# Performance work log

Hardware: AMD Instinct MI355X
Metric: run time of the kernel (lower is better)

The kernel has to match this reference:

```python
import jax, jax.numpy as jnp
import numpy as np

B, T, C, H, W = 16, 8, 2048, 16, 8
C8, C4, HW, NP = C // 8, C // 4, H * W, T // 2


def _cbr(x, w, s, b):
    # 1x1 conv + folded BN (eval-mode affine) + ReLU; x: (N, Cin, H, W), w: (Cout, Cin)
    y = jnp.einsum('oc,nchw->nohw', w, x)
    return jax.nn.relu(y * s[None, :, None, None] + b[None, :, None, None])


def setup_inputs():
    key = jax.random.key(0)
    ks = jax.random.split(key, 16)
    r = lambda i, shape, sc: jax.random.normal(ks[i], shape, jnp.float32) * sc
    return dict(
        featmap=r(0, (B, T, C, H, W), 1.0),
        re_featmap=r(1, (B * T, C, H, W), 1.0),
        vect_featmap=r(2, (B, T, C), 1.0),
        embed_feat=r(3, (B, T, 128, H, W), 1.0),
        gamma_w=r(4, (C8, C), 0.03), gamma_s=jnp.ones((C8,)), gamma_b=jnp.zeros((C8,)),
        beta_w=r(5, (C8, C), 0.03), beta_s=jnp.ones((C8,)), beta_b=jnp.zeros((C8,)),
        gg_w=r(6, (128, 2 * HW), 0.05), gg_s=jnp.ones((128,)), gg_b=jnp.zeros((128,)),
        tte_w=r(7, (128, 256), 0.05), tte_s=jnp.ones((128,)), tte_b=jnp.zeros((128,)),
        te_w=r(8, (1, 256), 0.05), te_s=jnp.ones((1,)), te_b=jnp.zeros((1,)),
        theta_w=r(9, (C8, C), 0.03), theta_b=jnp.zeros((C8,)),
        cp_w1=r(10, (C8, C4), 0.05), cp_b1=jnp.zeros((C8,)),
        cp_w2=r(11, (C, C8), 0.05), cp_b2=jnp.zeros((C,)),
    )


def reference(featmap, re_featmap, vect_featmap, embed_feat,
              gamma_w, gamma_s, gamma_b, beta_w, beta_s, beta_b,
              gg_w, gg_s, gg_b, tte_w, tte_s, tte_b, te_w, te_s, te_b,
              theta_w, theta_b, cp_w1, cp_b1, cp_w2, cp_b2):
    # spatial attention embeddings: (B, T, C8, HW)
    gamma = _cbr(re_featmap, gamma_w, gamma_s, gamma_b).reshape(B, T, C8, HW)
    beta = _cbr(re_featmap, beta_w, beta_s, beta_b).reshape(B, T, C8, HW)

    # channel attention: Conv1d over time of (B, C, T) -> (B, C8, T)
    cp = jax.nn.relu(jnp.einsum('oc,btc->bot', theta_w, vect_featmap) + theta_b[None, :, None])
    cp = cp.reshape(B, C8, NP, 2)
    c0 = cp[..., 0].transpose(0, 2, 1)  # (B, NP, C8)
    c1 = cp[..., 1].transpose(0, 2, 1)

    def mlp(x):  # (B, NP, C4) -> sigmoid gate (B, NP, C)
        h1 = jax.nn.relu(x @ cp_w1.T + cp_b1)
        return jax.nn.sigmoid(h1 @ cp_w2.T + cp_b2)

    p00 = mlp(jnp.concatenate([c0, c1], -1))  # (B, NP, C)
    p01 = mlp(jnp.concatenate([c1, c0], -1))

    # pairwise spatial graphs
    g0, g1 = gamma[:, 0::2], gamma[:, 1::2]  # (B, NP, C8, HW)
    b0, b1 = beta[:, 0::2], beta[:, 1::2]
    Gs0 = jnp.einsum('bpcs,bpct->bpst', g0, b1)  # (B, NP, HW, HW)
    Gs1 = jnp.einsum('bpcs,bpct->bpst', g1, b0)
    # Gs_in = Gs^T viewed as (HW, H, W); Gs_out = Gs viewed likewise
    j0 = jnp.concatenate([Gs0.transpose(0, 1, 3, 2), Gs1], 2).reshape(B * NP, 2 * HW, H, W)
    j1 = jnp.concatenate([Gs1.transpose(0, 1, 3, 2), Gs0], 2).reshape(B * NP, 2 * HW, H, W)
    gj0 = _cbr(j0, gg_w, gg_s, gg_b)  # (B*NP, 128, H, W)
    gj1 = _cbr(j1, gg_w, gg_s, gg_b)

    ef = embed_feat.reshape(B, NP, 2, 128, H, W)
    e0 = ef[:, :, 0].reshape(B * NP, 128, H, W)
    e1 = ef[:, :, 1].reshape(B * NP, 128, H, W)
    ta = _cbr(jnp.concatenate([e0, e1], 1), tte_w, tte_s, tte_b)  # (B*NP, 128, H, W)
    tb = _cbr(jnp.concatenate([e1, e0], 1), tte_w, tte_s, tte_b)

    def gate(t_feat, gj):  # conv 256->1 + BN + sigmoid
        y = jnp.einsum('oc,nchw->nohw', te_w, jnp.concatenate([t_feat, gj], 1))
        return jax.nn.sigmoid(y * te_s[None, :, None, None] + te_b[None, :, None, None])

    pa = gate(ta, gj0).reshape(B, NP, 1, H, W)
    pb = gate(tb, gj1).reshape(B, NP, 1, H, W)

    f = featmap.reshape(B, NP, 2, C, H, W)
    gate0 = p00[..., None, None] * pa  # (B, NP, C, H, W)
    gate1 = p01[..., None, None] * pb
    out = jax.nn.relu(gate0 * f[:, :, 0] + gate1 * f[:, :, 1])
    return out * out  # (B, T//2, C, H, W)
```

## Files before the change

kernel.cpp:

```cpp
#include <hip/hip_runtime.h>
#include <stdint.h>


typedef _Float16 f16;
typedef _Float16 f16x4 __attribute__((ext_vector_type(4)));
typedef _Float16 f16x8 __attribute__((ext_vector_type(8)));
typedef float f32x4 __attribute__((ext_vector_type(4)));

typedef const void __attribute__((address_space(1)))* gptr1;
typedef void __attribute__((address_space(3)))* lptr3;

__device__ __forceinline__ void gload16(const void* g, void* l) {
  __builtin_amdgcn_global_load_lds((gptr1)g, (lptr3)l, 16, 0, 0);
}

__device__ __forceinline__ float sigmoidf_(float x) { return 1.f / (1.f + expf(-x)); }

#define WAIT_VM6 asm volatile("s_waitcnt vmcnt(6)" ::: "memory")
#define WAIT_VM0 asm volatile("s_waitcnt vmcnt(0)" ::: "memory")
#define WAIT_LGKM8 asm volatile("s_waitcnt lgkmcnt(8)" ::: "memory")
#define WAIT_LGKM0 asm volatile("s_waitcnt lgkmcnt(0)" ::: "memory")

__global__ __launch_bounds__(256) void kPP(const float* __restrict__ x,
                                           f16* __restrict__ Af,
                                           const float* __restrict__ gw, const float* __restrict__ gs,
                                           const float* __restrict__ bw, const float* __restrict__ bs,
                                           const float* __restrict__ gg_w, const float* __restrict__ gg_s,
                                           const float* __restrict__ tte_w, const float* __restrict__ tte_s,
                                           const float* __restrict__ thw, const float* __restrict__ w1,
                                           const float* __restrict__ w2,
                                           f16* __restrict__ Wf,
                                           float* __restrict__ ggT, float* __restrict__ tteT,
                                           float* __restrict__ thwT, float* __restrict__ w1T,
                                           float* __restrict__ w2T) {
  __shared__ __align__(16) char shmem[64 * 129 * 4];
  int t = threadIdx.x;
  int bid = blockIdx.x;
  if (bid < 4096) {
    float (*L)[129] = (float(*)[129])shmem;
    int n = bid >> 5;
    int k0 = (bid & 31) * 64;
    const float* src = x + (size_t)n * 262144 + (size_t)k0 * 128;
    for (int r = 0; r < 8; ++r) {
      int f = r * 256 + t;
      int kk = f >> 5, c4 = (f & 31) * 4;
      float4 v = *(const float4*)(src + kk * 128 + c4);
      L[kk][c4 + 0] = v.x; L[kk][c4 + 1] = v.y; L[kk][c4 + 2] = v.z; L[kk][c4 + 3] = v.w;
    }
    __syncthreads();
    for (int r = 0; r < 4; ++r) {
      int id = r * 256 + t;
      int hw = id >> 3, c = id & 7;
      int cs = c ^ (hw & 7);
      f16x8 h8;
      for (int j = 0; j < 8; ++j)
        h8[j] = (f16)L[cs * 8 + j][hw];
      size_t m = (size_t)n * 128 + hw;
      size_t ob = m * 2048 + (size_t)k0 + (size_t)c * 8;
      *(f16x8*)(Af + ob) = h8;
    }
    return;
  }
  if (bid < 4608) {
    int id = (bid - 4096) * 256 + t;
    int o = id >> 8, cch = id & 255;
    float s; const float* row;
    if (o < 256) { s = gs[o]; row = gw + (size_t)o * 2048; }
    else         { s = bs[o - 256]; row = bw + (size_t)(o - 256) * 2048; }
    int kb = cch >> 3, sub = cch & 7;
    int subd = sub ^ (o & 7);
    f16x8 h8;
    for (int j = 0; j < 8; ++j)
      h8[j] = (f16)(row[cch * 8 + j] * s);
    size_t ob = (size_t)o * 2048 + (size_t)kb * 64 + (size_t)subd * 8;
    *(f16x8*)(Wf + ob) = h8;
    return;
  }
  float (*TL)[65] = (float(*)[65])shmem;
  int tb = bid - 4608;
  const float* src; float* dst; const float* scale = nullptr; int R, C;
  if (tb < 128)      { src = thw;   dst = thwT; R = 256;  C = 2048; }
  else if (tb < 256) { tb -= 128; src = w2;  dst = w2T;  R = 2048; C = 256; }
  else if (tb < 288) { tb -= 256; src = w1;  dst = w1T;  R = 256;  C = 512; }
  else if (tb < 296) { tb -= 288; src = gg_w;  dst = ggT;  scale = gg_s;  R = 128; C = 256; }
  else               { tb -= 296; src = tte_w; dst = tteT; scale = tte_s; R = 128; C = 256; }
  int tpc = C >> 6;
  int r0 = (tb / tpc) * 64, c0 = (tb % tpc) * 64;
  int i16 = t >> 4, j4 = (t & 15) * 4;
  for (int s = 0; s < 4; ++s) {
    int i = i16 + s * 16;
    float4 v = *(const float4*)(src + (size_t)(r0 + i) * C + c0 + j4);
    TL[i][j4 + 0] = v.x; TL[i][j4 + 1] = v.y; TL[i][j4 + 2] = v.z; TL[i][j4 + 3] = v.w;
  }
  __syncthreads();
  for (int s = 0; s < 4; ++s) {
    int j = i16 + s * 16;
    float4 w;
    w.x = TL[j4 + 0][j]; w.y = TL[j4 + 1][j]; w.z = TL[j4 + 2][j]; w.w = TL[j4 + 3][j];
    if (scale) {
      w.x *= scale[r0 + j4 + 0]; w.y *= scale[r0 + j4 + 1];
      w.z *= scale[r0 + j4 + 2]; w.w *= scale[r0 + j4 + 3];
    }
    *(float4*)(dst + (size_t)(c0 + j) * R + r0 + j4) = w;
  }
}

__global__ __launch_bounds__(512, 2) void kGemm8(const f16* __restrict__ Af, const f16* __restrict__ Wf,
                                                 const float* __restrict__ gamma_b, const float* __restrict__ beta_b,
                                                 f16* __restrict__ gammaFh, f16* __restrict__ betaFh) {
  __shared__ __align__(16) f16 S[3][24576];
  int t = threadIdx.x;
  int lane = t & 63, wid = t >> 6;
  int wr = wid >> 2, wc = wid & 3;
  int bid = blockIdx.x;
  int bx = (bid & 7) * 16 + (bid >> 4);
  int by = (bid >> 3) & 1;
  size_t M0 = (size_t)bx * 128;
  size_t N0 = (size_t)by * 256;
  int row8 = wid * 8 + (lane >> 3);
  int sl = lane & 7;
  int fr = lane & 15, fq = lane >> 4;
  f32x4 acc[4][4] = {};
  f16x8 a[8], b[8];

  const char* AB = (const char*)Af;
  const char* WB = (const char*)Wf;
  const size_t aoff0 = (M0 + row8) * 4096 + (size_t)sl * 16;
  const size_t aoff1 = (M0 + 64 + row8) * 4096 + (size_t)sl * 16;
  const size_t woff0 = (N0 + row8) * 4096 + (size_t)sl * 16;
  const size_t woff1 = (N0 + 64 + row8) * 4096 + (size_t)sl * 16;
  const size_t woff2 = (N0 + 128 + row8) * 4096 + (size_t)sl * 16;
  const size_t woff3 = (N0 + 192 + row8) * 4096 + (size_t)sl * 16;

#define STAGE_ALL(dst, s) do {                                                     \
    int koff_ = (s) << 7;                                                          \
    char* l_ = (char*)(dst) + wid * 1024;                                          \
    gload16(AB + aoff0 + koff_, l_);                                               \
    gload16(AB + aoff1 + koff_, l_ + 8192);                                        \
    gload16(WB + woff0 + koff_, l_ + 16384);                                       \
    gload16(WB + woff1 + koff_, l_ + 24576);                                       \
    gload16(WB + woff2 + koff_, l_ + 32768);                                       \
    gload16(WB + woff3 + koff_, l_ + 40960);                                       \
  } while (0)

#define LOADG(buf, g) do {                                                         \
    const f16* bA_ = (const f16*)(buf);                                            \
    const f16* bB_ = bA_ + 8192;                                                   \
    int cg_ = (g) * 4 + fq;                                                        \
    _Pragma("unroll") for (int mi = 0; mi < 4; ++mi) {                             \
      int m_ = wr * 64 + mi * 16 + fr;                                             \
      a[(g) * 4 + mi] = *(const f16x8*)(bA_ + m_ * 64 + ((cg_ ^ (m_ & 7)) << 3));  \
    }                                                                              \
    _Pragma("unroll") for (int ni = 0; ni < 4; ++ni) {                             \
      int n_ = wc * 64 + ni * 16 + fr;                                             \
      b[(g) * 4 + ni] = *(const f16x8*)(bB_ + n_ * 64 + ((cg_ ^ (n_ & 7)) << 3));  \
    }                                                                              \
  } while (0)

#define STEP(rdbuf, stbuf, kt) do {                                                \
    if ((kt) < 31) { WAIT_VM6; } else { WAIT_VM0; }                                \
    __builtin_amdgcn_s_barrier();                                                  \
    if ((kt) <= 29) STAGE_ALL(stbuf, (kt) + 2);                                    \
    LOADG(rdbuf, 0);                                                               \
    __builtin_amdgcn_sched_barrier(0);                                             \
    LOADG(rdbuf, 1);                                                               \
    WAIT_LGKM8;                                                                    \
    __builtin_amdgcn_sched_barrier(0);                                             \
    __builtin_amdgcn_s_setprio(1);                                                 \
    _Pragma("unroll") for (int mi = 0; mi < 4; ++mi)                               \
      _Pragma("unroll") for (int ni = 0; ni < 4; ++ni)                             \
        acc[mi][ni] = __builtin_amdgcn_mfma_f32_16x16x32_f16(a[mi], b[ni], acc[mi][ni], 0, 0, 0); \
    WAIT_LGKM0;                                                                    \
    __builtin_amdgcn_sched_barrier(0);                                             \
    _Pragma("unroll") for (int mi = 0; mi < 4; ++mi)                               \
      _Pragma("unroll") for (int ni = 0; ni < 4; ++ni)                             \
        acc[mi][ni] = __builtin_amdgcn_mfma_f32_16x16x32_f16(a[4 + mi], b[4 + ni], acc[mi][ni], 0, 0, 0); \
    __builtin_amdgcn_s_setprio(0);                                                 \
  } while (0)

  STAGE_ALL(&S[0][0], 0);
  STAGE_ALL(&S[1][0], 1);
  for (int base = 0; base < 30; base += 3) {
    STEP(&S[0][0], &S[2][0], base);
    STEP(&S[1][0], &S[0][0], base + 1);
    STEP(&S[2][0], &S[1][0], base + 2);
  }
  STEP(&S[0][0], &S[2][0], 30);
  STEP(&S[1][0], &S[0][0], 31);
#undef STEP
#undef LOADG
#undef STAGE_ALL

  const float* bias = by ? beta_b : gamma_b;
  f16* outb = by ? betaFh : gammaFh;
#pragma unroll
  for (int mi = 0; mi < 4; ++mi) {
    int hwb = wr * 64 + mi * 16 + fq * 4;
#pragma unroll
    for (int ni = 0; ni < 4; ++ni) {
      int o = wc * 64 + ni * 16 + fr;
      float bb = bias[o];
      f32x4 v = acc[mi][ni];
      f16x4 w;
      w[0] = (f16)fmaxf(v[0] + bb, 0.f);
      w[1] = (f16)fmaxf(v[1] + bb, 0.f);
      w[2] = (f16)fmaxf(v[2] + bb, 0.f);
      w[3] = (f16)fmaxf(v[3] + bb, 0.f);
      *(f16x4*)(outb + (size_t)bx * 32768 + (size_t)o * 128 + hwb) = w;
    }
  }
}

__global__ __launch_bounds__(256) void kTT(const float* __restrict__ vect, const float* __restrict__ thwT,
                                           float* __restrict__ P,
                                           const float* __restrict__ embed, const float* __restrict__ tteT,
                                           const float* __restrict__ tte_b, const float* __restrict__ te_w,
                                           float* __restrict__ Sta) {
  __shared__ float V[512];
  __shared__ __align__(16) float E[256 * 64];
  __shared__ float Red[16 * 64];
  int bid = blockIdx.x;
  int t = threadIdx.x;
  if (bid < 512) {
    int bt = bid & 127, kq = bid >> 7;
    const float* src = vect + (size_t)bt * 2048 + kq * 512;
    if (t < 128) *(float4*)(V + t * 4) = *(const float4*)(src + t * 4);
    __syncthreads();
    const float* wp = thwT + (size_t)kq * 512 * 256 + t;
    float acc = 0.f;
#pragma unroll 8
    for (int c = 0; c < 512; ++c)
      acc = fmaf(wp[(size_t)c * 256], V[c], acc);
    P[((size_t)kq * 128 + bt) * 256 + t] = acc;
    return;
  }
  int i = bid - 512;
  int n = i & 63, gate = (i >> 6) & 1, hh = (i >> 7) & 1;
  int b = n >> 2, p = n & 3;
  const float* eA = embed + (size_t)(b * 8 + 2 * p + gate) * 16384 + hh * 64;
  const float* eB = embed + (size_t)(b * 8 + 2 * p + 1 - gate) * 16384 + hh * 64;
  for (int r = 0; r < 8; ++r) {
    int f = r * 256 + t;
    int ch = f >> 4, q = (f & 15) * 4;
    *(float4*)(E + ch * 64 + q) = *(const float4*)(eA + (size_t)ch * 128 + q);
  }
  for (int r = 0; r < 8; ++r) {
    int f = r * 256 + t;
    int ch = f >> 4, q = (f & 15) * 4;
    *(float4*)(E + (128 + ch) * 64 + q) = *(const float4*)(eB + (size_t)ch * 128 + q);
  }
  __syncthreads();
  int ty = t >> 4, tx = t & 15;
  float acc[8][4] = {};
  for (int c = 0; c < 256; ++c) {
    float w8[8];
    *(float4*)w8 = *(const float4*)(tteT + (size_t)c * 128 + ty * 8);
    *(float4*)(w8 + 4) = *(const float4*)(tteT + (size_t)c * 128 + ty * 8 + 4);
    float4 g = *(const float4*)(E + c * 64 + tx * 4);
    for (int ii = 0; ii < 8; ++ii) {
      acc[ii][0] = fmaf(w8[ii], g.x, acc[ii][0]);
      acc[ii][1] = fmaf(w8[ii], g.y, acc[ii][1]);
      acc[ii][2] = fmaf(w8[ii], g.z, acc[ii][2]);
      acc[ii][3] = fmaf(w8[ii], g.w, acc[ii][3]);
    }
  }
  float par[4] = {0.f, 0.f, 0.f, 0.f};
  for (int ii = 0; ii < 8; ++ii) {
    int o = ty * 8 + ii;
    float tb = tte_b[o], tw = te_w[o];
    for (int j = 0; j < 4; ++j)
      par[j] += tw * fmaxf(acc[ii][j] + tb, 0.f);
  }
  for (int j = 0; j < 4; ++j) Red[ty * 64 + tx * 4 + j] = par[j];
  __syncthreads();
  if (t < 64) {
    float s = 0.f;
    for (int g = 0; g < 16; ++g) s += Red[g * 64 + t];
    Sta[(size_t)gate * 8192 + n * 128 + hh * 64 + t] = s;
  }
}

__global__ __launch_bounds__(256) void kAG(const float* __restrict__ P, const float* __restrict__ thb,
                                           const float* __restrict__ w1T, const float* __restrict__ b1,
                                           float* __restrict__ h1,
                                           const f16* __restrict__ gammaFh, const f16* __restrict__ betaFh,
                                           float* __restrict__ Gs0, float* __restrict__ Gs1) {
  __shared__ float x0[256], x1[256];
  __shared__ float ra[256], rb[256];
  __shared__ __align__(16) float As[16 * 128];
  __shared__ __align__(16) float Bs[16 * 64];
  int bid = blockIdx.x;
  int t = threadIdx.x;
  if (bid < 256) {
    int bp = bid & 63, och = bid >> 6;
    int b = bp >> 2, p = bp & 3;
    int bt0 = b * 8 + 2 * p, bt1 = bt0 + 1;
    {
      float a0 = 0.f, a1 = 0.f;
      for (int q = 0; q < 4; ++q) {
        a0 += P[((size_t)q * 128 + bt0) * 256 + t];
        a1 += P[((size_t)q * 128 + bt1) * 256 + t];
      }
      float tb = thb[t];
      x0[t] = fmaxf(a0 + tb, 0.f);
      x1[t] = fmaxf(a1 + tb, 0.f);
    }
    __syncthreads();
    int o = och * 64 + (t & 63);
    int ks = t >> 6;
    const float* xa = (ks < 2) ? x0 : x1;
    const float* xb = (ks < 2) ? x1 : x0;
    int kbase = ks * 128;
    int xoff = (ks < 2) ? kbase : kbase - 256;
    float aa = 0.f, ab = 0.f;
#pragma unroll 8
    for (int ii = 0; ii < 128; ++ii) {
      float w = w1T[(size_t)(kbase + ii) * 256 + o];
      aa = fmaf(w, xa[xoff + ii], aa);
      ab = fmaf(w, xb[xoff + ii], ab);
    }
    ra[t] = aa;
    rb[t] = ab;
    __syncthreads();
    if (t < 64) {
      float sa = ra[t] + ra[64 + t] + ra[128 + t] + ra[192 + t];
      float sb = rb[t] + rb[64 + t] + rb[128 + t] + rb[192 + t];
      float bb = b1[o];
      h1[((size_t)bp * 2) * 256 + o] = fmaxf(sa + bb, 0.f);
      h1[((size_t)bp * 2 + 1) * 256 + o] = fmaxf(sb + bb, 0.f);
    }
    return;
  }
  int i = bid - 256;
  int n = i & 63, which = (i >> 6) & 1, th = (i >> 7) & 1;
  int b = n >> 2, p = n & 3;
  int tg = 2 * p + which;
  int tb = 2 * p + 1 - which;
  const f16* A = gammaFh + (size_t)(b * 8 + tg) * 32768;
  const f16* Bm = betaFh + (size_t)(b * 8 + tb) * 32768;
  float* out = (which ? Gs1 : Gs0) + (size_t)n * 16384;
  int ty = t >> 4, tx = t & 15;
  float acc[8][4] = {};
  for (int c0 = 0; c0 < 256; c0 += 16) {
    {
      int cc = t >> 4, col8 = (t & 15) * 8;
      f16x8 v = *(const f16x8*)(A + (size_t)(c0 + cc) * 128 + col8);
      for (int j = 0; j < 8; ++j) As[cc * 128 + col8 + j] = (float)v[j];
    }
    if (t < 128) {
      int cc = t >> 3, col8 = (t & 7) * 8;
      f16x8 v = *(const f16x8*)(Bm + (size_t)(c0 + cc) * 128 + th * 64 + col8);
      for (int j = 0; j < 8; ++j) Bs[cc * 64 + col8 + j] = (float)v[j];
    }
    __syncthreads();
    for (int cc = 0; cc < 16; ++cc) {
      float a8[8];
      *(float4*)a8 = *(const float4*)(As + cc * 128 + ty * 8);
      *(float4*)(a8 + 4) = *(const float4*)(As + cc * 128 + ty * 8 + 4);
      float4 b4 = *(const float4*)(Bs + cc * 64 + tx * 4);
      for (int ii = 0; ii < 8; ++ii) {
        acc[ii][0] = fmaf(a8[ii], b4.x, acc[ii][0]);
        acc[ii][1] = fmaf(a8[ii], b4.y, acc[ii][1]);
        acc[ii][2] = fmaf(a8[ii], b4.z, acc[ii][2]);
        acc[ii][3] = fmaf(a8[ii], b4.w, acc[ii][3]);
      }
    }
    __syncthreads();
  }
  for (int ii = 0; ii < 8; ++ii) {
    *(float4*)(out + (size_t)(ty * 8 + ii) * 128 + th * 64 + tx * 4) =
        make_float4(acc[ii][0], acc[ii][1], acc[ii][2], acc[ii][3]);
  }
}

__global__ __launch_bounds__(256) void kBG(const float* __restrict__ h1, const float* __restrict__ w2T,
                                           const float* __restrict__ b2,
                                           float* __restrict__ p00, float* __restrict__ p01,
                                           const float* __restrict__ Gs0, const float* __restrict__ Gs1,
                                           const float* __restrict__ ggT, const float* __restrict__ gg_b,
                                           const float* __restrict__ te_w, float* __restrict__ Sgj) {
  __shared__ float ha[256], hb[256];
  __shared__ float G0h[64 * 129];
  __shared__ __align__(16) float G1c[128 * 64];
  __shared__ float Red[16 * 64];
  int bid = blockIdx.x;
  int t = threadIdx.x;
  if (bid < 512) {
    int bp = bid & 63, chc = bid >> 6;
    ha[t] = h1[((size_t)bp * 2) * 256 + t];
    hb[t] = h1[((size_t)bp * 2 + 1) * 256 + t];
    __syncthreads();
    int ch = chc * 256 + t;
    float sa = 0.f, sb = 0.f;
#pragma unroll 8
    for (int k = 0; k < 256; ++k) {
      float w = w2T[(size_t)k * 2048 + ch];
      sa = fmaf(w, ha[k], sa);
      sb = fmaf(w, hb[k], sb);
    }
    p00[(size_t)bp * 2048 + ch] = sigmoidf_(sa + b2[ch]);
    p01[(size_t)bp * 2048 + ch] = sigmoidf_(sb + b2[ch]);
    return;
  }
  int i = bid - 512;
  int n = i & 63, gate = (i >> 6) & 1, hh = (i >> 7) & 1;
  const float* srcT = (gate == 0 ? Gs0 : Gs1) + (size_t)n * 16384;
  const float* srcC = (gate == 0 ? Gs1 : Gs0) + (size_t)n * 16384;
  for (int r = 0; r < 8; ++r) {
    int f = r * 256 + t;
    int hwl = f >> 5, c4 = (f & 31) * 4;
    float4 v = *(const float4*)(srcT + (size_t)(hh * 64 + hwl) * 128 + c4);
    G0h[hwl * 129 + c4 + 0] = v.x;
    G0h[hwl * 129 + c4 + 1] = v.y;
    G0h[hwl * 129 + c4 + 2] = v.z;
    G0h[hwl * 129 + c4 + 3] = v.w;
  }
  for (int r = 0; r < 8; ++r) {
    int f = r * 256 + t;
    int c = f >> 4, q = (f & 15) * 4;
    *(float4*)(G1c + c * 64 + q) = *(const float4*)(srcC + (size_t)c * 128 + hh * 64 + q);
  }
  __syncthreads();
  int ty = t >> 4, tx = t & 15;
  float acc[8][4] = {};
  for (int c = 0; c < 128; ++c) {
    float w8[8];
    *(float4*)w8 = *(const float4*)(ggT + (size_t)c * 128 + ty * 8);
    *(float4*)(w8 + 4) = *(const float4*)(ggT + (size_t)c * 128 + ty * 8 + 4);
    float g4[4];
    for (int j = 0; j < 4; ++j) g4[j] = G0h[(tx * 4 + j) * 129 + c];
    for (int ii = 0; ii < 8; ++ii)
      for (int j = 0; j < 4; ++j)
        acc[ii][j] = fmaf(w8[ii], g4[j], acc[ii][j]);
  }
  for (int c = 0; c < 128; ++c) {
    float w8[8];
    *(float4*)w8 = *(const float4*)(ggT + (size_t)(128 + c) * 128 + ty * 8);
    *(float4*)(w8 + 4) = *(const float4*)(ggT + (size_t)(128 + c) * 128 + ty * 8 + 4);
    float4 g = *(const float4*)(G1c + c * 64 + tx * 4);
    for (int ii = 0; ii < 8; ++ii) {
      acc[ii][0] = fmaf(w8[ii], g.x, acc[ii][0]);
      acc[ii][1] = fmaf(w8[ii], g.y, acc[ii][1]);
      acc[ii][2] = fmaf(w8[ii], g.z, acc[ii][2]);
      acc[ii][3] = fmaf(w8[ii], g.w, acc[ii][3]);
    }
  }
  float par[4] = {0.f, 0.f, 0.f, 0.f};
  for (int ii = 0; ii < 8; ++ii) {
    int o = ty * 8 + ii;
    float gb = gg_b[o], tw = te_w[128 + o];
    for (int j = 0; j < 4; ++j)
      par[j] += tw * fmaxf(acc[ii][j] + gb, 0.f);
  }
  for (int j = 0; j < 4; ++j) Red[ty * 64 + tx * 4 + j] = par[j];
  __syncthreads();
  if (t < 64) {
    float s = 0.f;
    for (int g = 0; g < 16; ++g) s += Red[g * 64 + t];
    Sgj[(size_t)gate * 8192 + n * 128 + hh * 64 + t] = s;
  }
}

__global__ __launch_bounds__(256) void kFinal(const float* __restrict__ featmap, const float* __restrict__ p00,
                                              const float* __restrict__ p01, const float* __restrict__ Sta,
                                              const float* __restrict__ Sgj, const float* __restrict__ te_s,
                                              const float* __restrict__ te_b, float* __restrict__ out) {
  int fid = blockIdx.x * 256 + threadIdx.x;
  int h4 = (fid & 31) * 4;
  int c = (fid >> 5) & 2047;
  int bp = fid >> 16;
  int b = bp >> 2, p = bp & 3;
  float ga = p00[(size_t)bp * 2048 + c];
  float gb = p01[(size_t)bp * 2048 + c];
  float ts = te_s[0], tbv = te_b[0];
  float4 sa0 = *(const float4*)(Sta + (size_t)bp * 128 + h4);
  float4 sg0 = *(const float4*)(Sgj + (size_t)bp * 128 + h4);
  float4 sa1 = *(const float4*)(Sta + 8192 + (size_t)bp * 128 + h4);
  float4 sg1 = *(const float4*)(Sgj + 8192 + (size_t)bp * 128 + h4);
  float4 pa4, pb4;
  pa4.x = sigmoidf_(ts * (sa0.x + sg0.x) + tbv);
  pa4.y = sigmoidf_(ts * (sa0.y + sg0.y) + tbv);
  pa4.z = sigmoidf_(ts * (sa0.z + sg0.z) + tbv);
  pa4.w = sigmoidf_(ts * (sa0.w + sg0.w) + tbv);
  pb4.x = sigmoidf_(ts * (sa1.x + sg1.x) + tbv);
  pb4.y = sigmoidf_(ts * (sa1.y + sg1.y) + tbv);
  pb4.z = sigmoidf_(ts * (sa1.z + sg1.z) + tbv);
  pb4.w = sigmoidf_(ts * (sa1.w + sg1.w) + tbv);
  const float* f0 = featmap + (size_t)(b * 8 + 2 * p) * 262144 + (size_t)c * 128 + h4;
  const float* f1 = f0 + 262144;
  float4 v0 = *(const float4*)f0;
  float4 v1 = *(const float4*)f1;
  float4 o4;
  float r;
  r = fmaxf(ga * pa4.x * v0.x + gb * pb4.x * v1.x, 0.f); o4.x = r * r;
  r = fmaxf(ga * pa4.y * v0.y + gb * pb4.y * v1.y, 0.f); o4.y = r * r;
  r = fmaxf(ga * pa4.z * v0.z + gb * pb4.z * v1.z, 0.f); o4.z = r * r;
  r = fmaxf(ga * pa4.w * v0.w + gb * pb4.w * v1.w, 0.f); o4.w = r * r;
  *(float4*)(out + (size_t)fid * 4) = o4;
}

extern "C" void kernel_launch(void* const* d_in, const int* in_sizes, int n_in,
                              void* d_out, int out_size, void* d_ws, size_t ws_size,
                              hipStream_t stream) {
  (void)in_sizes; (void)n_in; (void)out_size; (void)ws_size;
  const float* featmap    = (const float*)d_in[0];
  const float* re_featmap = (const float*)d_in[1];
  const float* vect       = (const float*)d_in[2];
  const float* embed      = (const float*)d_in[3];
  const float* gamma_w    = (const float*)d_in[4];
  const float* gamma_s    = (const float*)d_in[5];
  const float* gamma_b    = (const float*)d_in[6];
  const float* beta_w     = (const float*)d_in[7];
  const float* beta_s     = (const float*)d_in[8];
  const float* beta_b     = (const float*)d_in[9];
  const float* gg_w       = (const float*)d_in[10];
  const float* gg_s       = (const float*)d_in[11];
  const float* gg_b       = (const float*)d_in[12];
  const float* tte_w      = (const float*)d_in[13];
  const float* tte_s      = (const float*)d_in[14];
  const float* tte_b      = (const float*)d_in[15];
  const float* te_w       = (const float*)d_in[16];
  const float* te_s       = (const float*)d_in[17];
  const float* te_b       = (const float*)d_in[18];
  const float* theta_w    = (const float*)d_in[19];
  const float* theta_b    = (const float*)d_in[20];
  const float* cp_w1      = (const float*)d_in[21];
  const float* cp_b1      = (const float*)d_in[22];
  const float* cp_w2      = (const float*)d_in[23];
  const float* cp_b2      = (const float*)d_in[24];
  float* out = (float*)d_out;

  char* w = (char*)d_ws;
  f16* Af  = (f16*)w;   w += (size_t)16384 * 2048 * 2;
  f16* Wf  = (f16*)w;   w += (size_t)512 * 2048 * 2;
  f16* gammaFh = (f16*)w; w += (size_t)128 * 256 * 128 * 2;
  f16* betaFh  = (f16*)w; w += (size_t)128 * 256 * 128 * 2;
  float* Gs0    = (float*)w; w += (size_t)64 * 128 * 128 * 4;
  float* Gs1    = (float*)w; w += (size_t)64 * 128 * 128 * 4;
  float* ggT    = (float*)w; w += (size_t)256 * 128 * 4;
  float* tteT   = (float*)w; w += (size_t)256 * 128 * 4;
  float* thwT   = (float*)w; w += (size_t)2048 * 256 * 4;
  float* w1T    = (float*)w; w += (size_t)512 * 256 * 4;
  float* w2T    = (float*)w; w += (size_t)256 * 2048 * 4;
  float* P      = (float*)w; w += (size_t)4 * 128 * 256 * 4;
  float* h1     = (float*)w; w += (size_t)64 * 2 * 256 * 4;
  float* Sta    = (float*)w; w += (size_t)2 * 64 * 128 * 4;
  float* Sgj    = (float*)w; w += (size_t)2 * 64 * 128 * 4;
  float* p00    = (float*)w; w += (size_t)64 * 2048 * 4;
  float* p01    = (float*)w; w += (size_t)64 * 2048 * 4;

  kPP<<<4912, 256, 0, stream>>>(re_featmap, Af,
                                gamma_w, gamma_s, beta_w, beta_s, gg_w, gg_s, tte_w, tte_s,
                                theta_w, cp_w1, cp_w2, Wf, ggT, tteT, thwT, w1T, w2T);
  kGemm8<<<256, 512, 0, stream>>>(Af, Wf, gamma_b, beta_b, gammaFh, betaFh);
  kTT<<<768, 256, 0, stream>>>(vect, thwT, P, embed, tteT, tte_b, te_w, Sta);
  kAG<<<512, 256, 0, stream>>>(P, theta_b, w1T, cp_b1, h1, gammaFh, betaFh, Gs0, Gs1);
  kBG<<<768, 256, 0, stream>>>(h1, w2T, cp_b2, p00, p01, Gs0, Gs1, ggT, gg_b, te_w, Sgj);
  kFinal<<<16384, 256, 0, stream>>>(featmap, p00, p01, Sta, Sgj, te_s, te_b, out);
}
```

Before: 245.6 us.

## Split transpose-cast blocks by spatial half and compute both tte gates per block

The kPP transpose/fp16-cast stage now covers half the spatial positions per block. This doubles the block count and shrinks the LDS tile from 64x129 to 64x65 floats, giving more parallelism and occupancy. In kTT, each block now loads the two embedding frames once and computes both gate directions (ta and tb) by reading tte weights with the channel halves swapped (c^128). This halves the embedding loads and the number of blocks. The trade-offs are more register pressure in kTT from doubled accumulators and more small blocks in kPP.

```diff
diff --git a/kernel.cpp b/kernel.cpp
--- a/kernel.cpp
+++ b/kernel.cpp
@@ -33,36 +33,38 @@
                                            float* __restrict__ ggT, float* __restrict__ tteT,
                                            float* __restrict__ thwT, float* __restrict__ w1T,
                                            float* __restrict__ w2T) {
-  __shared__ __align__(16) char shmem[64 * 129 * 4];
+  __shared__ __align__(16) char shmem[64 * 65 * 4];
   int t = threadIdx.x;
   int bid = blockIdx.x;
-  if (bid < 4096) {
-    float (*L)[129] = (float(*)[129])shmem;
-    int n = bid >> 5;
-    int k0 = (bid & 31) * 64;
-    const float* src = x + (size_t)n * 262144 + (size_t)k0 * 128;
-    for (int r = 0; r < 8; ++r) {
+  if (bid < 8192) {
+    float (*L)[65] = (float(*)[65])shmem;
+    int n = bid >> 6;
+    int kc = (bid >> 1) & 31;
+    int hh = bid & 1;
+    int k0 = kc * 64;
+    const float* src = x + (size_t)n * 262144 + (size_t)k0 * 128 + hh * 64;
+    for (int r = 0; r < 4; ++r) {
       int f = r * 256 + t;
-      int kk = f >> 5, c4 = (f & 31) * 4;
-      float4 v = *(const float4*)(src + kk * 128 + c4);
+      int kk = f >> 4, c4 = (f & 15) * 4;
+      float4 v = *(const float4*)(src + (size_t)kk * 128 + c4);
       L[kk][c4 + 0] = v.x; L[kk][c4 + 1] = v.y; L[kk][c4 + 2] = v.z; L[kk][c4 + 3] = v.w;
     }
     __syncthreads();
-    for (int r = 0; r < 4; ++r) {
+    for (int r = 0; r < 2; ++r) {
       int id = r * 256 + t;
       int hw = id >> 3, c = id & 7;
       int cs = c ^ (hw & 7);
       f16x8 h8;
       for (int j = 0; j < 8; ++j)
         h8[j] = (f16)L[cs * 8 + j][hw];
-      size_t m = (size_t)n * 128 + hw;
+      size_t m = (size_t)n * 128 + hh * 64 + hw;
       size_t ob = m * 2048 + (size_t)k0 + (size_t)c * 8;
       *(f16x8*)(Af + ob) = h8;
     }
     return;
   }
-  if (bid < 4608) {
-    int id = (bid - 4096) * 256 + t;
+  if (bid < 8704) {
+    int id = (bid - 8192) * 256 + t;
     int o = id >> 8, cch = id & 255;
     float s; const float* row;
     if (o < 256) { s = gs[o]; row = gw + (size_t)o * 2048; }
@@ -77,7 +79,7 @@
     return;
   }
   float (*TL)[65] = (float(*)[65])shmem;
-  int tb = bid - 4608;
+  int tb = bid - 8704;
   const float* src; float* dst; const float* scale = nullptr; int R, C;
   if (tb < 128)      { src = thw;   dst = thwT; R = 256;  C = 2048; }
   else if (tb < 256) { tb -= 128; src = w2;  dst = w2T;  R = 2048; C = 256; }
@@ -218,7 +220,7 @@
                                            float* __restrict__ Sta) {
   __shared__ float V[512];
   __shared__ __align__(16) float E[256 * 64];
-  __shared__ float Red[16 * 64];
+  __shared__ float Red2[2][16 * 64];
   int bid = blockIdx.x;
   int t = threadIdx.x;
   if (bid < 512) {
@@ -235,10 +237,10 @@
     return;
   }
   int i = bid - 512;
-  int n = i & 63, gate = (i >> 6) & 1, hh = (i >> 7) & 1;
+  int n = i & 63, hh = (i >> 6) & 1;
   int b = n >> 2, p = n & 3;
-  const float* eA = embed + (size_t)(b * 8 + 2 * p + gate) * 16384 + hh * 64;
-  const float* eB = embed + (size_t)(b * 8 + 2 * p + 1 - gate) * 16384 + hh * 64;
+  const float* eA = embed + (size_t)(b * 8 + 2 * p) * 16384 + hh * 64;
+  const float* eB = embed + (size_t)(b * 8 + 2 * p + 1) * 16384 + hh * 64;
   for (int r = 0; r < 8; ++r) {
     int f = r * 256 + t;
     int ch = f >> 4, q = (f & 15) * 4;
@@ -251,32 +253,46 @@
   }
   __syncthreads();
   int ty = t >> 4, tx = t & 15;
-  float acc[8][4] = {};
+  float acc0[8][4] = {}, acc1[8][4] = {};
   for (int c = 0; c < 256; ++c) {
-    float w8[8];
-    *(float4*)w8 = *(const float4*)(tteT + (size_t)c * 128 + ty * 8);
-    *(float4*)(w8 + 4) = *(const float4*)(tteT + (size_t)c * 128 + ty * 8 + 4);
+    float w8a[8], w8b[8];
+    *(float4*)w8a = *(const float4*)(tteT + (size_t)c * 128 + ty * 8);
+    *(float4*)(w8a + 4) = *(const float4*)(tteT + (size_t)c * 128 + ty * 8 + 4);
+    int c2 = c ^ 128;
+    *(float4*)w8b = *(const float4*)(tteT + (size_t)c2 * 128 + ty * 8);
+    *(float4*)(w8b + 4) = *(const float4*)(tteT + (size_t)c2 * 128 + ty * 8 + 4);
     float4 g = *(const float4*)(E + c * 64 + tx * 4);
     for (int ii = 0; ii < 8; ++ii) {
-      acc[ii][0] = fmaf(w8[ii], g.x, acc[ii][0]);
-      acc[ii][1] = fmaf(w8[ii], g.y, acc[ii][1]);
-      acc[ii][2] = fmaf(w8[ii], g.z, acc[ii][2]);
-      acc[ii][3] = fmaf(w8[ii], g.w, acc[ii][3]);
-    }
-  }
-  float par[4] = {0.f, 0.f, 0.f, 0.f};
+      acc0[ii][0] = fmaf(w8a[ii], g.x, acc0[ii][0]);
+      acc0[ii][1] = fmaf(w8a[ii], g.y, acc0[ii][1]);
+      acc0[ii][2] = fmaf(w8a[ii], g.z, acc0[ii][2]);
+      acc0[ii][3] = fmaf(w8a[ii], g.w, acc0[ii][3]);
+      acc1[ii][0] = fmaf(w8b[ii], g.x, acc1[ii][0]);
+      acc1[ii][1] = fmaf(w8b[ii], g.y, acc1[ii][1]);
+      acc1[ii][2] = fmaf(w8b[ii], g.z, acc1[ii][2]);
+      acc1[ii][3] = fmaf(w8b[ii], g.w, acc1[ii][3]);
+    }
+  }
+  float par0[4] = {0.f, 0.f, 0.f, 0.f};
+  float par1[4] = {0.f, 0.f, 0.f, 0.f};
   for (int ii = 0; ii < 8; ++ii) {
     int o = ty * 8 + ii;
     float tb = tte_b[o], tw = te_w[o];
-    for (int j = 0; j < 4; ++j)
-      par[j] += tw * fmaxf(acc[ii][j] + tb, 0.f);
-  }
-  for (int j = 0; j < 4; ++j) Red[ty * 64 + tx * 4 + j] = par[j];
+    for (int j = 0; j < 4; ++j) {
+      par0[j] += tw * fmaxf(acc0[ii][j] + tb, 0.f);
+      par1[j] += tw * fmaxf(acc1[ii][j] + tb, 0.f);
+    }
+  }
+  for (int j = 0; j < 4; ++j) {
+    Red2[0][ty * 64 + tx * 4 + j] = par0[j];
+    Red2[1][ty * 64 + tx * 4 + j] = par1[j];
+  }
   __syncthreads();
-  if (t < 64) {
+  if (t < 128) {
+    int g = t >> 6, tt = t & 63;
     float s = 0.f;
-    for (int g = 0; g < 16; ++g) s += Red[g * 64 + t];
-    Sta[(size_t)gate * 8192 + n * 128 + hh * 64 + t] = s;
+    for (int q = 0; q < 16; ++q) s += Red2[g][q * 64 + tt];
+    Sta[(size_t)g * 8192 + n * 128 + hh * 64 + tt] = s;
   }
 }
 
@@ -549,11 +565,11 @@
   float* p00    = (float*)w; w += (size_t)64 * 2048 * 4;
   float* p01    = (float*)w; w += (size_t)64 * 2048 * 4;
 
-  kPP<<<4912, 256, 0, stream>>>(re_featmap, Af,
+  kPP<<<9008, 256, 0, stream>>>(re_featmap, Af,
                                 gamma_w, gamma_s, beta_w, beta_s, gg_w, gg_s, tte_w, tte_s,
                                 theta_w, cp_w1, cp_w2, Wf, ggT, tteT, thwT, w1T, w2T);
   kGemm8<<<256, 512, 0, stream>>>(Af, Wf, gamma_b, beta_b, gammaFh, betaFh);
-  kTT<<<768, 256, 0, stream>>>(vect, thwT, P, embed, tteT, tte_b, te_w, Sta);
+  kTT<<<640, 256, 0, stream>>>(vect, thwT, P, embed, tteT, tte_b, te_w, Sta);
   kAG<<<512, 256, 0, stream>>>(P, theta_b, w1T, cp_b1, h1, gammaFh, betaFh, Gs0, Gs1);
   kBG<<<768, 256, 0, stream>>>(h1, w2T, cp_b2, p00, p01, Gs0, Gs1, ggT, gg_b, te_w, Sgj);
   kFinal<<<16384, 256, 0, stream>>>(featmap, p00, p01, Sta, Sgj, te_s, te_b, out);
```

Result: slower. 269.5 us (+9.7%).
